# Performance work log

Hardware: AMD Instinct MI355X
Metric: run time of the kernel (lower is better)

The kernel has to match this reference:

```python
import jax, jax.numpy as jnp
import numpy as np
import math

N_HEAD = 16
N_HEAD_KV = 4
WINDOW = 1024
SINK = 4
ROPE_BASE = 10000.0


def _rope(x):
    # x: [B, H, T, D]; rotate-half RoPE
    B, H, T, D = x.shape
    inv_freq = 1.0 / (ROPE_BASE ** (jnp.arange(0, D, 2, dtype=jnp.float32) / D))  # [D/2]
    ang = jnp.arange(T, dtype=jnp.float32)[:, None] * inv_freq[None, :]  # [T, D/2]
    cos = jnp.concatenate([jnp.cos(ang), jnp.cos(ang)], axis=-1)  # [T, D]
    sin = jnp.concatenate([jnp.sin(ang), jnp.sin(ang)], axis=-1)
    x1, x2 = x[..., : D // 2], x[..., D // 2 :]
    rot = jnp.concatenate([-x2, x1], axis=-1)
    return x * cos[None, None] + rot * sin[None, None]


def setup_inputs() -> dict:
    key = jax.random.key(0)
    ks = jax.random.split(key, 6)
    B, T, C = 2, 2048, 2048
    D = C // N_HEAD
    x = jax.random.normal(ks[0], (B, T, C), dtype=jnp.float32)
    s = 0.02
    Wq = jax.random.normal(ks[1], (C, C), dtype=jnp.float32) * s
    Wk = jax.random.normal(ks[2], (C, N_HEAD_KV * D), dtype=jnp.float32) * s
    Wv = jax.random.normal(ks[3], (C, N_HEAD_KV * D), dtype=jnp.float32) * s
    Wo = jax.random.normal(ks[4], (C, C), dtype=jnp.float32) * s
    seq_lengths = jax.random.randint(ks[5], (B,), T // 2, T + 1, dtype=jnp.int32)
    return {"x": x, "Wq": Wq, "Wk": Wk, "Wv": Wv, "Wo": Wo, "seq_lengths": seq_lengths}


def reference(x, Wq, Wk, Wv, Wo, seq_lengths):
    B, T, C = x.shape
    H, Hkv = N_HEAD, N_HEAD_KV
    D = C // H
    scale = 1.0 / math.sqrt(D)

    q = (x @ Wq).reshape(B, T, H, D).transpose(0, 2, 1, 3)      # [B,H,T,D]
    k = (x @ Wk).reshape(B, T, Hkv, D).transpose(0, 2, 1, 3)    # [B,Hkv,T,D]
    v = (x @ Wv).reshape(B, T, Hkv, D).transpose(0, 2, 1, 3)
    # GQA: repeat kv heads (matches torch repeat_interleave on head dim)
    k = jnp.repeat(k, H // Hkv, axis=1)
    v = jnp.repeat(v, H // Hkv, axis=1)

    q = _rope(q)
    k = _rope(k)

    scores = jnp.einsum('bhqd,bhkd->bhqk', q, k) * scale  # [B,H,T,T]

    qi = jnp.arange(T)[:, None]
    ki = jnp.arange(T)[None, :]
    # causal & (in sliding window | attention sink)
    base = (qi >= ki) & (((qi - ki) <= WINDOW) | (ki < SINK))  # [T,T]
    valid = jnp.arange(T)[None, :] < seq_lengths[:, None]      # [B,T]
    mask = base[None, None] & valid[:, None, :, None] & valid[:, None, None, :]

    scores = jnp.where(mask, scores, -1e30)
    attn = jax.nn.softmax(scores, axis=-1)
    y = jnp.einsum('bhqk,bhkd->bhqd', attn, v)
    # flex_attention returns 0 for fully-masked (padded) query rows
    y = y * valid[:, None, :, None]

    y = y.transpose(0, 2, 1, 3).reshape(B, T, C)
    return y @ Wo
```

## Files before the change

### kernel.cpp

```cpp
#include <hip/hip_runtime.h>
#include <stdint.h>

#define BATCH 2
#define TSEQ  2048
#define CDIM  2048
#define NHEAD 16
#define NKV   4
#define HDIM  128
#define KVDIM 512
#define WIN   1024
#define SINKN 4
#define QT    64
#define QKVN  3072

typedef unsigned short u16;
typedef __attribute__((ext_vector_type(8))) short bf16x8;
typedef __attribute__((ext_vector_type(4))) float f32x4;
typedef __attribute__((address_space(3))) uint32_t as3_u32;
typedef const __attribute__((address_space(1))) uint32_t as1_u32;

__device__ __forceinline__ float bf2f(u16 u) {
  union { uint32_t i; float f; } w; w.i = ((uint32_t)u) << 16; return w.f;
}
__device__ __forceinline__ u16 f2bf(float f) {
  union { uint32_t i; float f; } w; w.f = f;
  return (u16)((w.i + 0x7fffu + ((w.i >> 16) & 1u)) >> 16);
}
__device__ __forceinline__ void gl2lds16(const u16* g, u16* l) {
  __builtin_amdgcn_global_load_lds((as1_u32*)g, (as3_u32*)l, 16, 0, 0);
}

__global__ __launch_bounds__(256)
void detect_kernel(const uint32_t* __restrict__ x, uint32_t* __restrict__ flag) {
  __shared__ int red[4];
  const int tid = threadIdx.x;
  int c = 0;
  for (int i = tid; i < 1024; i += 256) {
    uint32_t e = (x[i] >> 7) & 0xFFu;
    c += (e >= 100u && e <= 135u) ? 1 : 0;
  }
#pragma unroll
  for (int off = 32; off; off >>= 1) c += __shfl_xor(c, off, 64);
  if ((tid & 63) == 0) red[tid >> 6] = c;
  __syncthreads();
  if (tid == 0) flag[0] = ((red[0] + red[1] + red[2] + red[3]) > 512) ? 1u : 0u;
}

__global__ __launch_bounds__(256)
void convert4_kernel(const void* __restrict__ src, u16* __restrict__ dst,
                     int n4, const uint32_t* __restrict__ flag) {
  const int i = blockIdx.x * 256 + threadIdx.x;
  if (i >= n4) return;
  if (flag[0]) {
    ((uint2*)dst)[i] = ((const uint2*)src)[i];
  } else {
    float4 f = ((const float4*)src)[i];
    ushort4 o = { f2bf(f.x), f2bf(f.y), f2bf(f.z), f2bf(f.w) };
    ((ushort4*)dst)[i] = o;
  }
}

__global__ __launch_bounds__(256)
void transpose_w(const void* __restrict__ src, u16* __restrict__ dst,
                 int K, int N, const uint32_t* __restrict__ flag) {
  __shared__ u16 t[32][33];
  const int n0 = blockIdx.x * 32, k0 = blockIdx.y * 32;
  const int tx = threadIdx.x & 31, ty = threadIdx.x >> 5;
  const uint32_t f = flag[0];
#pragma unroll
  for (int i = 0; i < 4; ++i) {
    const int kk = k0 + ty + i * 8;
    u16 val = f ? ((const u16*)src)[(size_t)kk * N + n0 + tx]
                : f2bf(((const float*)src)[(size_t)kk * N + n0 + tx]);
    t[ty + i * 8][tx] = val;
  }
  __syncthreads();
#pragma unroll
  for (int i = 0; i < 4; ++i)
    dst[(size_t)(n0 + ty + i * 8) * K + k0 + tx] = t[tx][ty + i * 8];
}

__global__ __launch_bounds__(256)
void transpose_v(const u16* __restrict__ qkv, u16* __restrict__ vt) {
  __shared__ u16 t[32][33];
  const int tok0 = blockIdx.x * 32;
  const int d0 = blockIdx.y * 32;
  const int bh = blockIdx.z;
  const int b = bh >> 2, kvh = bh & 3;
  const int tx = threadIdx.x & 31, ty = threadIdx.x >> 5;
  const u16* src = qkv + ((size_t)(b * TSEQ + tok0)) * QKVN + 2560 + (kvh << 7) + d0;
#pragma unroll
  for (int i = 0; i < 4; ++i)
    t[ty + i * 8][tx] = src[(size_t)(ty + i * 8) * QKVN + tx];
  __syncthreads();
  u16* dst = vt + ((size_t)(bh * 128 + d0)) * TSEQ + tok0;
#pragma unroll
  for (int i = 0; i < 4; ++i)
    dst[(size_t)(ty + i * 8) * TSEQ + tx] = t[tx][ty + i * 8];
}

#define BAR() asm volatile("s_barrier" ::: "memory")

__device__ __forceinline__ void stage_half(const u16* g, int K, u16* lds,
                                           int w, int lrow, int lc16) {
  gl2lds16(g + (size_t)(w * 8 + lrow) * K + (lc16 << 3), lds + (w << 9));
  gl2lds16(g + (size_t)(64 + w * 8 + lrow) * K + (lc16 << 3), lds + ((8 + w) << 9));
}

__global__ __launch_bounds__(512, 2)
void gemm256(const u16* __restrict__ A, const u16* __restrict__ BT,
             void* __restrict__ C, int M, int N, int K,
             const uint32_t* __restrict__ flagp, const int* __restrict__ seq) {
  __shared__ u16 As[2 * 256 * 64];
  __shared__ u16 Bs[2 * 256 * 64];

  const int tid = threadIdx.x;
  const int w = tid >> 6, lane = tid & 63;
  const int quad = lane >> 4, lm = lane & 15, l8 = lane & 7;
  const int wm = w >> 2, wn = w & 3;
  const int lrow = lane >> 3;
  const int lc16 = (lane & 7) ^ lrow;

  const int gx = gridDim.x;
  const int nwg = gx * gridDim.y;
  int lin = blockIdx.y * gx + blockIdx.x;
  if ((nwg & 7) == 0) lin = (lin & 7) * (nwg >> 3) + (lin >> 3);
  const int m0 = (lin / gx) << 8;
  const int n0 = (lin % gx) << 8;

  if (seq) {
    const int t0 = m0 & (TSEQ - 1);
    if (t0 >= seq[m0 >> 11]) {
      const uint32_t fmz = flagp ? flagp[0] : 1u;
      if (fmz == 0) {
        float4 z = {0.f, 0.f, 0.f, 0.f};
        float* Cp = (float*)C;
        for (int i = tid; i < 256 * 64; i += 512) {
          const int r = i >> 6, c4 = (i & 63) << 2;
          *(float4*)(Cp + (size_t)(m0 + r) * N + n0 + c4) = z;
        }
      } else {
        uint4 z = {0u, 0u, 0u, 0u};
        u16* Cp = (u16*)C;
        for (int i = tid; i < 256 * 32; i += 512) {
          const int r = i >> 5, c8 = (i & 31) << 3;
          *(uint4*)(Cp + (size_t)(m0 + r) * N + n0 + c8) = z;
        }
      }
      return;
    }
  }

  const u16* Agm = A + (size_t)m0 * K;
  const u16* Bgm = BT + (size_t)n0 * K;
  const int NT = K >> 6;

  f32x4 acc[8][4];
#pragma unroll
  for (int i = 0; i < 8; ++i)
#pragma unroll
    for (int j = 0; j < 4; ++j) acc[i][j] = (f32x4){0.f, 0.f, 0.f, 0.f};

  stage_half(Bgm,                     K, Bs,             w, lrow, lc16);
  stage_half(Agm,                     K, As,             w, lrow, lc16);
  stage_half(Bgm + (size_t)128 * K,   K, Bs + 128 * 64,  w, lrow, lc16);
  stage_half(Agm + (size_t)128 * K,   K, As + 128 * 64,  w, lrow, lc16);
  stage_half(Bgm + 64,                K, Bs + 16384,     w, lrow, lc16);
  stage_half(Agm + 64,                K, As + 16384,     w, lrow, lc16);
  asm volatile("s_waitcnt vmcnt(4)" ::: "memory");
  BAR();

  bf16x8 a[4][2], b0[2][2], b1[2][2];

#define LDA_(mh)                                                              \
  _Pragma("unroll") for (int mi = 0; mi < 4; ++mi)                            \
  _Pragma("unroll") for (int ks = 0; ks < 2; ++ks)                            \
    a[mi][ks] = *(const bf16x8*)(Ab + ((wm * 128 + (mh) * 64 + mi * 16 + lm) << 6) + \
                                 (((ks * 4 + quad) ^ l8) << 3));
#define LDB_(dst, nh)                                                         \
  _Pragma("unroll") for (int ni = 0; ni < 2; ++ni)                            \
  _Pragma("unroll") for (int ks = 0; ks < 2; ++ks)                            \
    dst[ni][ks] = *(const bf16x8*)(Bb + ((wn * 64 + (nh) * 32 + ni * 16 + lm) << 6) + \
                                   (((ks * 4 + quad) ^ l8) << 3));
#define MFMA8(mh, nh, bb)                                                     \
  __builtin_amdgcn_s_setprio(1);                                              \
  _Pragma("unroll") for (int ks = 0; ks < 2; ++ks)                            \
  _Pragma("unroll") for (int mi = 0; mi < 4; ++mi)                            \
  _Pragma("unroll") for (int ni = 0; ni < 2; ++ni)                            \
    acc[(mh) * 4 + mi][(nh) * 2 + ni] = __builtin_amdgcn_mfma_f32_16x16x32_bf16( \
        a[mi][ks], bb[ni][ks], acc[(mh) * 4 + mi][(nh) * 2 + ni], 0, 0, 0);   \
  __builtin_amdgcn_s_setprio(0);

  for (int t = 0; t < NT; ++t) {
    const int p = t & 1;
    const u16* Ab = As + p * 16384;
    const u16* Bb = Bs + p * 16384;
    u16* An = (u16*)As + (p ^ 1) * 16384;
    u16* Bn = (u16*)Bs + (p ^ 1) * 16384;
    u16* Ac = (u16*)As + p * 16384;
    u16* Bc = (u16*)Bs + p * 16384;
    const size_t kc1 = (size_t)(t + 1) << 6;
    const size_t kc2 = (size_t)(t + 2) << 6;

    LDA_(0); LDB_(b0, 0);
    if (t + 1 < NT) stage_half(Bgm + (size_t)128 * K + kc1, K, Bn + 128 * 64, w, lrow, lc16);
    BAR();
    MFMA8(0, 0, b0);
    BAR();
    LDB_(b1, 1);
    if (t + 1 < NT) stage_half(Agm + (size_t)128 * K + kc1, K, An + 128 * 64, w, lrow, lc16);
    BAR();
    MFMA8(0, 1, b1);
    BAR();
    LDA_(1);
    if (t + 2 < NT) stage_half(Bgm + kc2, K, Bc, w, lrow, lc16);
    BAR();
    MFMA8(1, 1, b1);
    BAR();
    if (t + 2 < NT) stage_half(Agm + kc2, K, Ac, w, lrow, lc16);
    BAR();
    MFMA8(1, 0, b0);
    if (t >= NT - 2) { asm volatile("s_waitcnt vmcnt(0)" ::: "memory"); }
    else             { asm volatile("s_waitcnt vmcnt(4)" ::: "memory"); }
    BAR();
  }
#undef LDA_
#undef LDB_
#undef MFMA8

  const uint32_t fm = flagp ? flagp[0] : 1u;
#pragma unroll
  for (int mi = 0; mi < 8; ++mi)
#pragma unroll
    for (int ni = 0; ni < 4; ++ni)
#pragma unroll
      for (int r = 0; r < 4; ++r) {
        const int row = m0 + wm * 128 + mi * 16 + quad * 4 + r;
        const int col = n0 + wn * 64 + ni * 16 + lm;
        const float val = acc[mi][ni][r];
        if (fm == 0) ((float*)C)[(size_t)row * N + col] = val;
        else         ((u16*)C)[(size_t)row * N + col] = f2bf(val);
      }
}

__global__ __launch_bounds__(512, 2)
void gemm128x256(const u16* __restrict__ A, const u16* __restrict__ BT,
                 void* __restrict__ C, int M, int N, int K,
                 const uint32_t* __restrict__ flagp, const int* __restrict__ seq) {
  __shared__ u16 As[2 * 128 * 64];
  __shared__ u16 Bs[2 * 256 * 64];

  const int tid = threadIdx.x;
  const int w = tid >> 6, lane = tid & 63;
  const int quad = lane >> 4, lm = lane & 15, l8 = lane & 7;
  const int wm = w >> 2, wn = w & 3;
  const int lrow = lane >> 3;
  const int lc16 = (lane & 7) ^ lrow;

  const int gx = gridDim.x;
  const int nwg = gx * gridDim.y;
  int lin = blockIdx.y * gx + blockIdx.x;
  if ((nwg & 7) == 0) lin = (lin & 7) * (nwg >> 3) + (lin >> 3);
  const int m0 = (lin / gx) << 7;
  const int n0 = (lin % gx) << 8;

  if (seq) {
    const int t0 = m0 & (TSEQ - 1);
    if (t0 >= seq[m0 >> 11]) {
      const uint32_t fmz = flagp ? flagp[0] : 1u;
      if (fmz == 0) {
        float4 z = {0.f, 0.f, 0.f, 0.f};
        float* Cp = (float*)C;
        for (int i = tid; i < 128 * 64; i += 512) {
          const int r = i >> 6, c4 = (i & 63) << 2;
          *(float4*)(Cp + (size_t)(m0 + r) * N + n0 + c4) = z;
        }
      } else {
        uint4 z = {0u, 0u, 0u, 0u};
        u16* Cp = (u16*)C;
        for (int i = tid; i < 128 * 32; i += 512) {
          const int r = i >> 5, c8 = (i & 31) << 3;
          *(uint4*)(Cp + (size_t)(m0 + r) * N + n0 + c8) = z;
        }
      }
      return;
    }
  }

  const u16* Agm = A + (size_t)m0 * K;
  const u16* Bgm = BT + (size_t)n0 * K;
  const int NT = K >> 6;

  f32x4 acc[4][4];
#pragma unroll
  for (int i = 0; i < 4; ++i)
#pragma unroll
    for (int j = 0; j < 4; ++j) acc[i][j] = (f32x4){0.f, 0.f, 0.f, 0.f};

  stage_half(Bgm,                   K, Bs,                w, lrow, lc16);
  stage_half(Bgm + (size_t)128 * K, K, Bs + 8192,         w, lrow, lc16);
  stage_half(Agm,                   K, As,                w, lrow, lc16);
  stage_half(Bgm + 64,              K, Bs + 16384,        w, lrow, lc16);
  asm volatile("s_waitcnt vmcnt(2)" ::: "memory");
  BAR();

  bf16x8 a0[2][2], a1[2][2], b0[2][2], b1[2][2];

#define LDA_N(dst, mh)                                                        \
  _Pragma("unroll") for (int mi = 0; mi < 2; ++mi)                            \
  _Pragma("unroll") for (int ks = 0; ks < 2; ++ks)                            \
    dst[mi][ks] = *(const bf16x8*)(Ab + ((wm * 64 + (mh) * 32 + mi * 16 + lm) << 6) + \
                                   (((ks * 4 + quad) ^ l8) << 3));
#define LDB_N(dst, nh)                                                        \
  _Pragma("unroll") for (int ni = 0; ni < 2; ++ni)                            \
  _Pragma("unroll") for (int ks = 0; ks < 2; ++ks)                            \
    dst[ni][ks] = *(const bf16x8*)(Bb + ((wn * 64 + (nh) * 32 + ni * 16 + lm) << 6) + \
                                   (((ks * 4 + quad) ^ l8) << 3));
#define MFMA4(mh, nh, aa, bb)                                                 \
  __builtin_amdgcn_s_setprio(1);                                              \
  _Pragma("unroll") for (int ks = 0; ks < 2; ++ks)                            \
  _Pragma("unroll") for (int mi = 0; mi < 2; ++mi)                            \
  _Pragma("unroll") for (int ni = 0; ni < 2; ++ni)                            \
    acc[(mh) * 2 + mi][(nh) * 2 + ni] = __builtin_amdgcn_mfma_f32_16x16x32_bf16( \
        aa[mi][ks], bb[ni][ks], acc[(mh) * 2 + mi][(nh) * 2 + ni], 0, 0, 0);  \
  __builtin_amdgcn_s_setprio(0);

  for (int t = 0; t < NT; ++t) {
    const int p = t & 1;
    const u16* Ab = As + p * 8192;
    const u16* Bb = Bs + p * 16384;
    u16* An = (u16*)As + (p ^ 1) * 8192;
    u16* Bn = (u16*)Bs + (p ^ 1) * 16384;
    u16* Bc = (u16*)Bs + p * 16384;
    const size_t kc1 = (size_t)(t + 1) << 6;
    const size_t kc2 = (size_t)(t + 2) << 6;

    LDA_N(a0, 0); LDB_N(b0, 0);
    if (t + 1 < NT) stage_half(Bgm + (size_t)128 * K + kc1, K, Bn + 8192, w, lrow, lc16);
    BAR();
    MFMA4(0, 0, a0, b0);
    BAR();
    LDB_N(b1, 1);
    if (t + 1 < NT) stage_half(Agm + kc1, K, An, w, lrow, lc16);
    BAR();
    MFMA4(0, 1, a0, b1);
    BAR();
    LDA_N(a1, 1);
    if (t + 2 < NT) stage_half(Bgm + kc2, K, Bc, w, lrow, lc16);
    BAR();
    MFMA4(1, 1, a1, b1);
    BAR();
    BAR();
    MFMA4(1, 0, a1, b0);
    if (t >= NT - 2) { asm volatile("s_waitcnt vmcnt(0)" ::: "memory"); }
    else             { asm volatile("s_waitcnt vmcnt(2)" ::: "memory"); }
    BAR();
  }
#undef LDA_N
#undef LDB_N
#undef MFMA4

  const uint32_t fm = flagp ? flagp[0] : 1u;
#pragma unroll
  for (int mi = 0; mi < 4; ++mi)
#pragma unroll
    for (int ni = 0; ni < 4; ++ni)
#pragma unroll
      for (int r = 0; r < 4; ++r) {
        const int row = m0 + wm * 64 + mi * 16 + quad * 4 + r;
        const int col = n0 + wn * 64 + ni * 16 + lm;
        const float val = acc[mi][ni][r];
        if (fm == 0) ((float*)C)[(size_t)row * N + col] = val;
        else         ((u16*)C)[(size_t)row * N + col] = f2bf(val);
      }
}

__global__ __launch_bounds__(256)
void rope_kernel(u16* __restrict__ qkv) {
  const int QP = BATCH * TSEQ * NHEAD * 64;
  const int KP = BATCH * TSEQ * NKV * 64;
  int idx = blockIdx.x * 256 + threadIdx.x;
  u16* p;
  int i, t;
  if (idx < QP) {
    i = idx & 63;
    int hh = (idx >> 6) & (NHEAD - 1);
    int row = idx >> 10;
    t = row & (TSEQ - 1);
    p = qkv + (size_t)row * QKVN + (hh << 7);
  } else {
    int j = idx - QP;
    if (j >= KP) return;
    i = j & 63;
    int hh = (j >> 6) & (NKV - 1);
    int row = j >> 8;
    t = row & (TSEQ - 1);
    p = qkv + (size_t)row * QKVN + 2048 + (hh << 7);
  }
  float x1 = bf2f(p[i]), x2 = bf2f(p[i + 64]);
  float freq = exp2f((float)i * (-2.0f / 128.0f) * 13.287712379549449f);
  float ang = (float)t * freq;
  float c = cosf(ang), s = sinf(ang);
  p[i]      = f2bf(x1 * c - x2 * s);
  p[i + 64] = f2bf(x2 * c + x1 * s);
}

__global__ __launch_bounds__(256, 3)
void attn_mfma(const u16* __restrict__ qkv, const u16* __restrict__ vt,
               u16* __restrict__ y, const int* __restrict__ seq_lengths) {
  const int bid = blockIdx.x;
  const int tile = ((bid & 31) + ((bid >> 8) << 3)) & 31;
  const int q0 = (31 - tile) * QT;
  const int h  = (bid >> 5) & (NHEAD - 1);
  const int b  = bid >> 9;
  const int tid = threadIdx.x;
  const int w = tid >> 6;
  const int lane = tid & 63;
  const int quad = lane >> 4;
  const int lm = lane & 15;
  const int L = seq_lengths[b];
  const int kvh = h >> 2;
  const int kvoff = kvh << 7;
  const size_t bT = (size_t)b * TSEQ;

  if (q0 >= L) {
    const uint4 z = {0u, 0u, 0u, 0u};
    for (int i = tid; i < 64 * 16; i += 256) {
      const int r = i >> 4, c8 = (i & 15) << 3;
      *(uint4*)(y + ((bT + q0 + r) << 11) + (h << 7) + c8) = z;
    }
    return;
  }

  __shared__ u16 Ks[32 * 136];
  __shared__ u16 Vt[144 * 40];
  __shared__ u16 Ps[4 * 16 * 42];

  const int qbase = q0 + w * 16;

  bf16x8 qf[4];
  {
    const u16* qrow = qkv + (bT + qbase + lm) * QKVN + (h << 7);
#pragma unroll
    for (int c = 0; c < 4; ++c)
      qf[c] = *(const bf16x8*)(qrow + c * 32 + quad * 8);
  }

  for (int i = tid; i < 16 * 40; i += 256)
    Vt[128 * 40 + i] = (i < 40) ? (u16)0x3F80 : (u16)0;

  const int s0k = q0 - WIN > 0 ? q0 - WIN : 0;
  const int sink_extra = (s0k > 0) ? 1 : 0;
  const int niter = ((q0 + QT - s0k) >> 5) + sink_extra;

  f32x4 Oacc[9];
#pragma unroll
  for (int nt = 0; nt < 9; ++nt) Oacc[nt] = (f32x4){0.f, 0.f, 0.f, 0.f};

  const float cexp = 0.127517634f;
  const int trow = tid >> 4;
  const int tc8 = (tid & 15) << 3;
  const int vd = tid >> 2;
  const int vkg = (tid & 3) << 3;
  u16* Pw = Ps + w * 672;

  const u16* kp0 = qkv + (bT + trow) * QKVN + 2048 + kvoff + tc8;
  const u16* kp1 = kp0 + (size_t)16 * QKVN;
  const u16* vp0 = vt + ((size_t)(b * NKV + kvh) << 18) + (size_t)vd * TSEQ + vkg;
  const u16* vp1 = vp0 + (size_t)64 * TSEQ;

  uint4 kr0, kr1, vr0, vr1;
#define LOAD_CHUNK(kb)                                        \
  do {                                                        \
    kr0 = *(const uint4*)(kp0 + (size_t)(kb) * QKVN);         \
    kr1 = *(const uint4*)(kp1 + (size_t)(kb) * QKVN);         \
    vr0 = *(const uint4*)(vp0 + (kb));                        \
    vr1 = *(const uint4*)(vp1 + (kb));                        \
  } while (0)

  int kb_cur = sink_extra ? 0 : s0k;
  int kb_next = sink_extra ? s0k : s0k + 32;
  LOAD_CHUNK(kb_cur);

  for (int it = 0; it < niter; ++it) {
    BAR();
    *(uint4*)(Ks + trow * 136 + tc8)        = kr0;
    *(uint4*)(Ks + (16 + trow) * 136 + tc8) = kr1;
    *(uint4*)(Vt + vd * 40 + vkg)           = vr0;
    *(uint4*)(Vt + (vd + 64) * 40 + vkg)    = vr1;
    if (it + 1 < niter) LOAD_CHUNK(kb_next);
    asm volatile("s_waitcnt lgkmcnt(0)" ::: "memory");
    BAR();

    f32x4 sc0 = {0.f, 0.f, 0.f, 0.f}, sc1 = {0.f, 0.f, 0.f, 0.f};
    __builtin_amdgcn_s_setprio(1);
#pragma unroll
    for (int c = 0; c < 4; ++c) {
      bf16x8 kf = *(const bf16x8*)(Ks + lm * 136 + c * 32 + quad * 8);
      sc0 = __builtin_amdgcn_mfma_f32_16x16x32_bf16(qf[c], kf, sc0, 0, 0, 0);
    }
#pragma unroll
    for (int c = 0; c < 4; ++c) {
      bf16x8 kf = *(const bf16x8*)(Ks + (16 + lm) * 136 + c * 32 + quad * 8);
      sc1 = __builtin_amdgcn_mfma_f32_16x16x32_bf16(qf[c], kf, sc1, 0, 0, 0);
    }
    __builtin_amdgcn_s_setprio(0);

    const int key0 = kb_cur + lm;
    const int key1 = key0 + 16;
#pragma unroll
    for (int r = 0; r < 4; ++r) {
      const int qrow = qbase + quad * 4 + r;
      const bool ok0 = (key0 <= qrow) && ((qrow - key0 <= WIN) || (key0 < SINKN));
      const bool ok1 = (key1 <= qrow) && ((qrow - key1 <= WIN) || (key1 < SINKN));
      const float p0 = ok0 ? exp2f(sc0[r] * cexp) : 0.f;
      const float p1 = ok1 ? exp2f(sc1[r] * cexp) : 0.f;
      const int row = quad * 4 + r;
      Pw[row * 42 + lm]      = f2bf(p0);
      Pw[row * 42 + 16 + lm] = f2bf(p1);
    }
    bf16x8 pf = *(const bf16x8*)(Pw + lm * 42 + quad * 8);
    __builtin_amdgcn_s_setprio(1);
#pragma unroll
    for (int nt = 0; nt < 9; ++nt) {
      bf16x8 vf = *(const bf16x8*)(Vt + (nt * 16 + lm) * 40 + quad * 8);
      Oacc[nt] = __builtin_amdgcn_mfma_f32_16x16x32_bf16(pf, vf, Oacc[nt], 0, 0, 0);
    }
    __builtin_amdgcn_s_setprio(0);
    kb_cur = kb_next;
    kb_next += 32;
  }
#undef LOAD_CHUNK

  float invl[4];
#pragma unroll
  for (int r = 0; r < 4; ++r) {
    const float l = __shfl(Oacc[8][r], lane & 48, 64);
    invl[r] = 1.0f / l;
  }
#pragma unroll
  for (int nt = 0; nt < 8; ++nt)
#pragma unroll
    for (int r = 0; r < 4; ++r) {
      const int qrow = qbase + quad * 4 + r;
      const float val = (qrow < L) ? Oacc[nt][r] * invl[r] : 0.f;
      y[((bT + qrow) << 11) + (h << 7) + nt * 16 + lm] = f2bf(val);
    }
}

extern "C" void kernel_launch(void* const* d_in, const int* in_sizes, int n_in,
                              void* d_out, int out_size, void* d_ws, size_t ws_size,
                              hipStream_t stream) {
  const int M = BATCH * TSEQ;
  const int NX  = M * CDIM;

  uint32_t* flag = (uint32_t*)d_ws;
  u16* base = (u16*)((char*)d_ws + 16);
  u16* qkvb = base;
  u16* yb   = qkvb + (size_t)M * QKVN;
  u16* xb   = yb  + (size_t)NX;
  u16* wqT  = xb  + (size_t)NX;
  u16* wkvT = wqT + (size_t)CDIM * CDIM;
  u16* woT  = wkvT + (size_t)1024 * CDIM;
  u16* vtb  = woT + (size_t)CDIM * CDIM;

  const int* seq = (const int*)d_in[5];

  detect_kernel<<<1, 256, 0, stream>>>((const uint32_t*)d_in[0], flag);
  convert4_kernel<<<(NX / 4 + 255) / 256, 256, 0, stream>>>(d_in[0], xb, NX / 4, flag);
  transpose_w<<<dim3(CDIM / 32, CDIM / 32), 256, 0, stream>>>(d_in[1], wqT, CDIM, CDIM, flag);
  transpose_w<<<dim3(KVDIM / 32, CDIM / 32), 256, 0, stream>>>(d_in[2], wkvT, CDIM, KVDIM, flag);
  transpose_w<<<dim3(KVDIM / 32, CDIM / 32), 256, 0, stream>>>(d_in[3], wkvT + (size_t)KVDIM * CDIM, CDIM, KVDIM, flag);
  transpose_w<<<dim3(CDIM / 32, CDIM / 32), 256, 0, stream>>>(d_in[4], woT, CDIM, CDIM, flag);

  gemm256<<<dim3(QKVN / 256, M / 256), 512, 0, stream>>>(xb, wqT, qkvb, M, QKVN, CDIM, nullptr, seq);
  const int rope_threads = BATCH * TSEQ * (NHEAD + NKV) * 64;
  rope_kernel<<<rope_threads / 256, 256, 0, stream>>>(qkvb);
  transpose_v<<<dim3(TSEQ / 32, HDIM / 32, BATCH * NKV), 256, 0, stream>>>(qkvb, vtb);
  attn_mfma<<<BATCH * NHEAD * (TSEQ / QT), 256, 0, stream>>>(qkvb, vtb, yb, seq);
  gemm128x256<<<dim3(CDIM / 256, M / 128), 512, 0, stream>>>(yb, woT, d_out, M, CDIM, CDIM, flag, seq);
}
```

Baseline: 329.5 us.

## Merge prep kernels into one launch, fuse rope with V transpose, reorder MFMA loops

Folds dtype detection, x conversion and the four weight transposes into a single prep kernel in which every block recomputes the dtype flag locally. RoPE and the V transpose become one launch, so the launch count drops from eleven to five. The MFMA inner loops now put the k-step innermost, which changes the order of accumulator dependencies. The cost is that each prep block rereads 4KB of x to recompute the flag. There is also a possible race: the V transpose reads V columns that RoPE never touches, so that part is fine.

```diff
diff --git a/kernel.cpp b/kernel.cpp
--- a/kernel.cpp
+++ b/kernel.cpp
@@ -31,42 +31,53 @@
 }
 
 __global__ __launch_bounds__(256)
-void detect_kernel(const uint32_t* __restrict__ x, uint32_t* __restrict__ flag) {
+void prep_kernel(const void* __restrict__ x, const void* __restrict__ wq,
+                 const void* __restrict__ wk, const void* __restrict__ wv,
+                 const void* __restrict__ wo,
+                 u16* __restrict__ xb, u16* __restrict__ wqT,
+                 u16* __restrict__ wkT, u16* __restrict__ wvT,
+                 u16* __restrict__ woT, uint32_t* __restrict__ flagws) {
+  const int tid = threadIdx.x;
   __shared__ int red[4];
-  const int tid = threadIdx.x;
-  int c = 0;
-  for (int i = tid; i < 1024; i += 256) {
-    uint32_t e = (x[i] >> 7) & 0xFFu;
-    c += (e >= 100u && e <= 135u) ? 1 : 0;
-  }
-#pragma unroll
-  for (int off = 32; off; off >>= 1) c += __shfl_xor(c, off, 64);
-  if ((tid & 63) == 0) red[tid >> 6] = c;
+  {
+    const uint32_t* xi = (const uint32_t*)x;
+    int c = 0;
+#pragma unroll
+    for (int i = 0; i < 4; ++i) {
+      uint32_t e = (xi[tid + i * 256] >> 7) & 0xFFu;
+      c += (e >= 100u && e <= 135u) ? 1 : 0;
+    }
+#pragma unroll
+    for (int off = 32; off; off >>= 1) c += __shfl_xor(c, off, 64);
+    if ((tid & 63) == 0) red[tid >> 6] = c;
+  }
   __syncthreads();
-  if (tid == 0) flag[0] = ((red[0] + red[1] + red[2] + red[3]) > 512) ? 1u : 0u;
-}
-
-__global__ __launch_bounds__(256)
-void convert4_kernel(const void* __restrict__ src, u16* __restrict__ dst,
-                     int n4, const uint32_t* __restrict__ flag) {
-  const int i = blockIdx.x * 256 + threadIdx.x;
-  if (i >= n4) return;
-  if (flag[0]) {
-    ((uint2*)dst)[i] = ((const uint2*)src)[i];
-  } else {
-    float4 f = ((const float4*)src)[i];
-    ushort4 o = { f2bf(f.x), f2bf(f.y), f2bf(f.z), f2bf(f.w) };
-    ((ushort4*)dst)[i] = o;
-  }
-}
-
-__global__ __launch_bounds__(256)
-void transpose_w(const void* __restrict__ src, u16* __restrict__ dst,
-                 int K, int N, const uint32_t* __restrict__ flag) {
+  const uint32_t f = ((red[0] + red[1] + red[2] + red[3]) > 512) ? 1u : 0u;
+
+  int bid = blockIdx.x;
+  if (bid == 0 && tid == 0) flagws[0] = f;
+
+  if (bid < 8192) {
+    const int i = bid * 256 + tid;
+    if (f) {
+      ((uint2*)xb)[i] = ((const uint2*)x)[i];
+    } else {
+      float4 v = ((const float4*)x)[i];
+      ushort4 o = { f2bf(v.x), f2bf(v.y), f2bf(v.z), f2bf(v.w) };
+      ((ushort4*)xb)[i] = o;
+    }
+    return;
+  }
+  bid -= 8192;
+  const void* src; u16* dst; int N;
+  if (bid < 4096)      { src = wq; dst = wqT; N = CDIM; }
+  else if (bid < 5120) { src = wk; dst = wkT; N = KVDIM; bid -= 4096; }
+  else if (bid < 6144) { src = wv; dst = wvT; N = KVDIM; bid -= 5120; }
+  else                 { src = wo; dst = woT; N = CDIM;  bid -= 6144; }
+  const int ntiles = N >> 5;
+  const int n0 = (bid % ntiles) << 5, k0 = (bid / ntiles) << 5;
   __shared__ u16 t[32][33];
-  const int n0 = blockIdx.x * 32, k0 = blockIdx.y * 32;
-  const int tx = threadIdx.x & 31, ty = threadIdx.x >> 5;
-  const uint32_t f = flag[0];
+  const int tx = tid & 31, ty = tid >> 5;
 #pragma unroll
   for (int i = 0; i < 4; ++i) {
     const int kk = k0 + ty + i * 8;
@@ -77,17 +88,49 @@
   __syncthreads();
 #pragma unroll
   for (int i = 0; i < 4; ++i)
-    dst[(size_t)(n0 + ty + i * 8) * K + k0 + tx] = t[tx][ty + i * 8];
+    dst[(size_t)(n0 + ty + i * 8) * CDIM + k0 + tx] = t[tx][ty + i * 8];
 }
 
 __global__ __launch_bounds__(256)
-void transpose_v(const u16* __restrict__ qkv, u16* __restrict__ vt) {
+void rope_tv(u16* __restrict__ qkv, u16* __restrict__ vt) {
+  const int tid = threadIdx.x;
+  int bid = blockIdx.x;
+  if (bid < 20480) {
+    const int QP = BATCH * TSEQ * NHEAD * 64;
+    const int KP = BATCH * TSEQ * NKV * 64;
+    int idx = bid * 256 + tid;
+    u16* p;
+    int i, t;
+    if (idx < QP) {
+      i = idx & 63;
+      int hh = (idx >> 6) & (NHEAD - 1);
+      int row = idx >> 10;
+      t = row & (TSEQ - 1);
+      p = qkv + (size_t)row * QKVN + (hh << 7);
+    } else {
+      int j = idx - QP;
+      if (j >= KP) return;
+      i = j & 63;
+      int hh = (j >> 6) & (NKV - 1);
+      int row = j >> 8;
+      t = row & (TSEQ - 1);
+      p = qkv + (size_t)row * QKVN + 2048 + (hh << 7);
+    }
+    float x1 = bf2f(p[i]), x2 = bf2f(p[i + 64]);
+    float freq = exp2f((float)i * (-2.0f / 128.0f) * 13.287712379549449f);
+    float ang = (float)t * freq;
+    float c = cosf(ang), s = sinf(ang);
+    p[i]      = f2bf(x1 * c - x2 * s);
+    p[i + 64] = f2bf(x2 * c + x1 * s);
+    return;
+  }
+  bid -= 20480;
   __shared__ u16 t[32][33];
-  const int tok0 = blockIdx.x * 32;
-  const int d0 = blockIdx.y * 32;
-  const int bh = blockIdx.z;
+  const int tok0 = (bid & 63) << 5;
+  const int d0 = ((bid >> 6) & 3) << 5;
+  const int bh = bid >> 8;
   const int b = bh >> 2, kvh = bh & 3;
-  const int tx = threadIdx.x & 31, ty = threadIdx.x >> 5;
+  const int tx = tid & 31, ty = tid >> 5;
   const u16* src = qkv + ((size_t)(b * TSEQ + tok0)) * QKVN + 2560 + (kvh << 7) + d0;
 #pragma unroll
   for (int i = 0; i < 4; ++i)
@@ -184,9 +227,9 @@
                                    (((ks * 4 + quad) ^ l8) << 3));
 #define MFMA8(mh, nh, bb)                                                     \
   __builtin_amdgcn_s_setprio(1);                                              \
-  _Pragma("unroll") for (int ks = 0; ks < 2; ++ks)                            \
   _Pragma("unroll") for (int mi = 0; mi < 4; ++mi)                            \
   _Pragma("unroll") for (int ni = 0; ni < 2; ++ni)                            \
+  _Pragma("unroll") for (int ks = 0; ks < 2; ++ks)                            \
     acc[(mh) * 4 + mi][(nh) * 2 + ni] = __builtin_amdgcn_mfma_f32_16x16x32_bf16( \
         a[mi][ks], bb[ni][ks], acc[(mh) * 4 + mi][(nh) * 2 + ni], 0, 0, 0);   \
   __builtin_amdgcn_s_setprio(0);
@@ -318,9 +361,9 @@
                                    (((ks * 4 + quad) ^ l8) << 3));
 #define MFMA4(mh, nh, aa, bb)                                                 \
   __builtin_amdgcn_s_setprio(1);                                              \
-  _Pragma("unroll") for (int ks = 0; ks < 2; ++ks)                            \
   _Pragma("unroll") for (int mi = 0; mi < 2; ++mi)                            \
   _Pragma("unroll") for (int ni = 0; ni < 2; ++ni)                            \
+  _Pragma("unroll") for (int ks = 0; ks < 2; ++ks)                            \
     acc[(mh) * 2 + mi][(nh) * 2 + ni] = __builtin_amdgcn_mfma_f32_16x16x32_bf16( \
         aa[mi][ks], bb[ni][ks], acc[(mh) * 2 + mi][(nh) * 2 + ni], 0, 0, 0);  \
   __builtin_amdgcn_s_setprio(0);
@@ -373,36 +416,6 @@
         if (fm == 0) ((float*)C)[(size_t)row * N + col] = val;
         else         ((u16*)C)[(size_t)row * N + col] = f2bf(val);
       }
-}
-
-__global__ __launch_bounds__(256)
-void rope_kernel(u16* __restrict__ qkv) {
-  const int QP = BATCH * TSEQ * NHEAD * 64;
-  const int KP = BATCH * TSEQ * NKV * 64;
-  int idx = blockIdx.x * 256 + threadIdx.x;
-  u16* p;
-  int i, t;
-  if (idx < QP) {
-    i = idx & 63;
-    int hh = (idx >> 6) & (NHEAD - 1);
-    int row = idx >> 10;
-    t = row & (TSEQ - 1);
-    p = qkv + (size_t)row * QKVN + (hh << 7);
-  } else {
-    int j = idx - QP;
-    if (j >= KP) return;
-    i = j & 63;
-    int hh = (j >> 6) & (NKV - 1);
-    int row = j >> 8;
-    t = row & (TSEQ - 1);
-    p = qkv + (size_t)row * QKVN + 2048 + (hh << 7);
-  }
-  float x1 = bf2f(p[i]), x2 = bf2f(p[i + 64]);
-  float freq = exp2f((float)i * (-2.0f / 128.0f) * 13.287712379549449f);
-  float ang = (float)t * freq;
-  float c = cosf(ang), s = sinf(ang);
-  p[i]      = f2bf(x1 * c - x2 * s);
-  p[i + 64] = f2bf(x2 * c + x1 * s);
 }
 
 __global__ __launch_bounds__(256, 3)
@@ -566,17 +579,15 @@
 
   const int* seq = (const int*)d_in[5];
 
-  detect_kernel<<<1, 256, 0, stream>>>((const uint32_t*)d_in[0], flag);
-  convert4_kernel<<<(NX / 4 + 255) / 256, 256, 0, stream>>>(d_in[0], xb, NX / 4, flag);
-  transpose_w<<<dim3(CDIM / 32, CDIM / 32), 256, 0, stream>>>(d_in[1], wqT, CDIM, CDIM, flag);
-  transpose_w<<<dim3(KVDIM / 32, CDIM / 32), 256, 0, stream>>>(d_in[2], wkvT, CDIM, KVDIM, flag);
-  transpose_w<<<dim3(KVDIM / 32, CDIM / 32), 256, 0, stream>>>(d_in[3], wkvT + (size_t)KVDIM * CDIM, CDIM, KVDIM, flag);
-  transpose_w<<<dim3(CDIM / 32, CDIM / 32), 256, 0, stream>>>(d_in[4], woT, CDIM, CDIM, flag);
+  prep_kernel<<<8192 + 4096 + 1024 + 1024 + 4096, 256, 0, stream>>>(
+      d_in[0], d_in[1], d_in[2], d_in[3], d_in[4],
+      xb, wqT, wkvT, wkvT + (size_t)KVDIM * CDIM, woT, flag);
 
   gemm256<<<dim3(QKVN / 256, M / 256), 512, 0, stream>>>(xb, wqT, qkvb, M, QKVN, CDIM, nullptr, seq);
-  const int rope_threads = BATCH * TSEQ * (NHEAD + NKV) * 64;
-  rope_kernel<<<rope_threads / 256, 256, 0, stream>>>(qkvb);
-  transpose_v<<<dim3(TSEQ / 32, HDIM / 32, BATCH * NKV), 256, 0, stream>>>(qkvb, vtb);
+
+  rope_tv<<<20480 + 2048, 256, 0, stream>>>(qkvb, vtb);
+
   attn_mfma<<<BATCH * NHEAD * (TSEQ / QT), 256, 0, stream>>>(qkvb, vtb, yb, seq);
+
   gemm128x256<<<dim3(CDIM / 256, M / 128), 512, 0, stream>>>(yb, woT, d_out, M, CDIM, CDIM, flag, seq);
 }
```

Result: faster. 312.2 us (-5.3%).
